# Performance work log

Measured on AMD Instinct MI355X. Metric: run time of the kernel, lower is better.

## Reference

```python
import jax, jax.numpy as jnp
import numpy as np

N = 50000
E = 1600000
F_IN = 503
F_H = 128
NEG_SLOPE = 0.2


def setup_inputs() -> dict:
    key = jax.random.key(0)
    ks = jax.random.split(key, 24)
    s = 0.05
    inp = {
        "x": jax.random.normal(ks[0], (N, F_IN), jnp.float32),
        "edge_index": jax.random.randint(ks[1], (2, E), 0, N, jnp.int64),
        "edge_attr": jax.random.uniform(ks[2], (E, 1), jnp.float32),
        "input_mask": jax.random.uniform(ks[3], (N, 1), jnp.float32),
        # GATConv layer 1 (in=503, out=128, heads=1, edge_dim=1)
        "W1": jax.random.normal(ks[4], (F_IN, F_H), jnp.float32) * s,
        "b1": jnp.zeros((F_H,), jnp.float32),
        "as1": jax.random.normal(ks[5], (F_H,), jnp.float32) * s,
        "ad1": jax.random.normal(ks[6], (F_H,), jnp.float32) * s,
        "We1": jax.random.normal(ks[7], (1, F_H), jnp.float32) * s,
        "ae1": jax.random.normal(ks[8], (F_H,), jnp.float32) * s,
        # GATConv layer 2 (in=128, out=128)
        "W2": jax.random.normal(ks[9], (F_H, F_H), jnp.float32) * s,
        "b2": jnp.zeros((F_H,), jnp.float32),
        "as2": jax.random.normal(ks[10], (F_H,), jnp.float32) * s,
        "ad2": jax.random.normal(ks[11], (F_H,), jnp.float32) * s,
        "We2": jax.random.normal(ks[12], (1, F_H), jnp.float32) * s,
        "ae2": jax.random.normal(ks[13], (F_H,), jnp.float32) * s,
        # edge/node heads
        "Wb": jax.random.normal(ks[14], (F_H, 1), jnp.float32) * s,
        "bb": jnp.zeros((1,), jnp.float32),
        "Ww": jax.random.normal(ks[15], (F_H, 1), jnp.float32) * s,
        "bw": jnp.zeros((1,), jnp.float32),
    }
    return inp


def _gat_conv(x, src, dst, ea, W, b, a_src_vec, a_dst_vec, We, a_edge_vec):
    """PyG GATConv, heads=1, add_self_loops=True, fill_value='mean'."""
    n = x.shape[0]
    loop = jnp.arange(n)
    # self-loop edge attrs = mean of incoming edge attrs (0 if none)
    deg = jax.ops.segment_sum(jnp.ones(dst.shape, ea.dtype), dst, num_segments=n)
    ea_loop = jax.ops.segment_sum(ea, dst, num_segments=n) / jnp.maximum(deg, 1.0)[:, None]
    s = jnp.concatenate([src, loop])
    d = jnp.concatenate([dst, loop])
    ea2 = jnp.concatenate([ea, ea_loop], axis=0)  # [E+N, 1]

    h = x @ W                              # [N, F_H]
    a_s = h @ a_src_vec                    # [N]
    a_d = h @ a_dst_vec                    # [N]
    a_e = (ea2 @ We) @ a_edge_vec          # [E+N]

    alpha = jax.nn.leaky_relu(a_s[s] + a_d[d] + a_e, NEG_SLOPE)
    # scatter-softmax over destination neighborhoods (every node has a self loop)
    m = jax.lax.stop_gradient(jax.ops.segment_max(alpha, d, num_segments=n))
    ex = jnp.exp(alpha - m[d])
    den = jax.ops.segment_sum(ex, d, num_segments=n)
    coef = ex / den[d]                     # [E+N]

    out = jax.ops.segment_sum(coef[:, None] * h[s], d, num_segments=n)
    return out + b


def reference(x, edge_index, edge_attr, input_mask,
              W1, b1, as1, ad1, We1, ae1,
              W2, b2, as2, ad2, We2, ae2,
              Wb, bb, Ww, bw):
    src, dst = edge_index[0], edge_index[1]
    h = jax.nn.relu(_gat_conv(x, src, dst, edge_attr, W1, b1, as1, ad1, We1, ae1))
    h = jax.nn.relu(_gat_conv(h, src, dst, edge_attr, W2, b2, as2, ad2, We2, ae2))
    b_out = (h @ Wb + bb) * input_mask          # [N, 1]
    # directed graph: is_directed() is True, so use all edges
    w = ((h[src] + h[dst]) * 0.5) @ Ww + bw     # [E, 1]
    return (w, b_out)
```

## Files before the change

kernel.cpp:

```cpp
#include <hip/hip_runtime.h>
#include <hip/hip_fp16.h>

#define FH 128
#define NEG_SLOPE 0.2f
#define GBM 64
#define GBK 64

typedef _Float16 f16x8 __attribute__((ext_vector_type(8)));
typedef float f32x4 __attribute__((ext_vector_type(4)));

__global__ void rank_kernel(const int* __restrict__ ei, int* __restrict__ cnt,
                            unsigned short* __restrict__ rank, int E) {
  int e = blockIdx.x * 256 + threadIdx.x;
  if (e >= E) return;
  int dst = ei[E + e];
  rank[e] = (unsigned short)atomicAdd(&cnt[dst], 1);
}

__global__ void scan_blocksum(const int* __restrict__ deg, int* __restrict__ bsum, int n) {
  __shared__ int sm[256];
  int i = blockIdx.x * 256 + threadIdx.x;
  sm[threadIdx.x] = (i < n) ? deg[i] : 0;
  __syncthreads();
  for (int off = 128; off > 0; off >>= 1) {
    if (threadIdx.x < off) sm[threadIdx.x] += sm[threadIdx.x + off];
    __syncthreads();
  }
  if (threadIdx.x == 0) bsum[blockIdx.x] = sm[0];
}

__global__ void scan_bsum(int* __restrict__ bsum, int nb, int* __restrict__ rowptr, int N) {
  __shared__ int sm[1024];
  int t = threadIdx.x;
  int v = (t < nb) ? bsum[t] : 0;
  sm[t] = v;
  __syncthreads();
  for (int off = 1; off < 1024; off <<= 1) {
    int u = (t >= off) ? sm[t - off] : 0;
    __syncthreads();
    sm[t] += u;
    __syncthreads();
  }
  if (t < nb) bsum[t] = sm[t] - v;
  if (t == 1023) rowptr[N] = sm[1023];
}

__global__ void scan_final(const int* __restrict__ deg, const int* __restrict__ bsum,
                           int* __restrict__ rowptr, int n) {
  __shared__ int sm[256];
  int i = blockIdx.x * 256 + threadIdx.x;
  int v = (i < n) ? deg[i] : 0;
  sm[threadIdx.x] = v;
  __syncthreads();
  for (int off = 1; off < 256; off <<= 1) {
    int u = (threadIdx.x >= off) ? sm[threadIdx.x - off] : 0;
    __syncthreads();
    sm[threadIdx.x] += u;
    __syncthreads();
  }
  if (i < n) rowptr[i] = bsum[blockIdx.x] + sm[threadIdx.x] - v;
}

__global__ void place_kernel(const int* __restrict__ ei, const float* __restrict__ ea,
                             const int* __restrict__ rowptr,
                             const unsigned short* __restrict__ rank,
                             unsigned int* __restrict__ pack, int E) {
  int e = blockIdx.x * 256 + threadIdx.x;
  if (e >= E) return;
  int src = ei[e], dst = ei[E + e];
  int pos = rowptr[dst] + rank[e];
  unsigned short h = __half_as_ushort(__float2half(ea[e]));
  pack[pos] = ((unsigned int)src << 16) | h;
}

__global__ void cvec_kernel(const float* __restrict__ We1, const float* __restrict__ ae1,
                            const float* __restrict__ We2, const float* __restrict__ ae2,
                            float* __restrict__ cv) {
  int l = threadIdx.x;
  float s1 = We1[l] * ae1[l] + We1[l + 64] * ae1[l + 64];
  float s2 = We2[l] * ae2[l] + We2[l + 64] * ae2[l + 64];
  for (int off = 32; off; off >>= 1) { s1 += __shfl_down(s1, off); s2 += __shfl_down(s2, off); }
  if (l == 0) { cv[0] = s1; cv[1] = s2; }
}

__global__ void wcvt_kernel(const float* __restrict__ W, __half* __restrict__ Wt,
                            int K, int Kpad) {
  int idx = blockIdx.x * 256 + threadIdx.x;
  if (idx >= 128 * Kpad) return;
  int n = idx / Kpad, k = idx - n * Kpad;
  Wt[idx] = (k < K) ? __float2half(W[(size_t)k * 128 + n]) : __float2half(0.f);
}

__global__ __launch_bounds__(256, 4) void mfma_gemm_kernel(
    const float* __restrict__ X, const __half* __restrict__ Wt_,
    const float* __restrict__ avs, const float* __restrict__ avd,
    __half* __restrict__ H16, float* __restrict__ a_s, float* __restrict__ a_d,
    int M, int K, int Kpad) {
  __shared__ _Float16 Bl[2 * 8 * 64 * 8];
  const _Float16* __restrict__ Wt = (const _Float16*)Wt_;
  const int tid  = threadIdx.x;
  const int lane = tid & 63;
  const int w    = tid >> 6;
  const int m0   = blockIdx.x * GBM;

  f32x4 acc[8];
  #pragma unroll
  for (int i = 0; i < 8; i++) acc[i] = (f32x4){0.f, 0.f, 0.f, 0.f};

  const int arow   = m0 + w * 16 + (lane & 15);
  const int arow_c = arow < M ? arow : (M - 1);
  const float* __restrict__ Xrow = X + (size_t)arow_c * K;
  const int kgrp = (lane >> 4) * 8;

  const int sg = tid & 7, snb = tid >> 3;

  for (int k0 = 0; k0 < Kpad; k0 += GBK) {
    #pragma unroll
    for (int i = 0; i < 4; i++) {
      int n = snb + 32 * i;
      f16x8 v = *(const f16x8*)(Wt + (size_t)n * Kpad + k0 + sg * 8);
      int kt = sg >> 2, nt = n >> 4;
      int fl = (n & 15) + (sg & 3) * 16;
      *(f16x8*)&Bl[((kt * 8 + nt) * 64 + fl) * 8] = v;
    }
    __syncthreads();
    const bool fast = (k0 + GBK <= K);
    #pragma unroll
    for (int kt = 0; kt < 2; kt++) {
      int kb = k0 + kt * 32 + kgrp;
      f16x8 af;
      if (fast) {
        #pragma unroll
        for (int j = 0; j < 8; j++) af[j] = (_Float16)Xrow[kb + j];
      } else {
        #pragma unroll
        for (int j = 0; j < 8; j++)
          af[j] = (kb + j < K) ? (_Float16)Xrow[kb + j] : (_Float16)0.f;
      }
      #pragma unroll
      for (int nt = 0; nt < 8; nt++) {
        f16x8 bf = *(const f16x8*)&Bl[((kt * 8 + nt) * 64 + lane) * 8];
        acc[nt] = __builtin_amdgcn_mfma_f32_16x16x32_f16(af, bf, acc[nt], 0, 0, 0);
      }
    }
    __syncthreads();
  }

  const int rbase = m0 + w * 16 + (lane >> 4) * 4;
  const int col   = lane & 15;
  float as_v[8], ad_v[8];
  #pragma unroll
  for (int nt = 0; nt < 8; nt++) {
    as_v[nt] = avs[nt * 16 + col];
    ad_v[nt] = avd[nt * 16 + col];
  }
  #pragma unroll
  for (int r = 0; r < 4; r++) {
    int gm = rbase + r;
    float ps = 0.f, pd = 0.f;
    #pragma unroll
    for (int nt = 0; nt < 8; nt++) {
      ps += acc[nt][r] * as_v[nt];
      pd += acc[nt][r] * ad_v[nt];
    }
    #pragma unroll
    for (int msk = 1; msk < 16; msk <<= 1) {
      ps += __shfl_xor(ps, msk);
      pd += __shfl_xor(pd, msk);
    }
    if (gm < M) {
      #pragma unroll
      for (int nt = 0; nt < 8; nt++)
        H16[(size_t)gm * FH + nt * 16 + col] = __float2half(acc[nt][r]);
      if (col == 0) { a_s[gm] = ps; a_d[gm] = pd; }
    }
  }
}

__global__ __launch_bounds__(256) void agg_kernel(
    const __half* __restrict__ H16, const int* __restrict__ rowptr,
    const unsigned int* __restrict__ pack,
    const float* __restrict__ a_s, const float* __restrict__ a_d,
    const float* __restrict__ cv, int cidx,
    const float* __restrict__ bias,
    float* __restrict__ Hout, int N) {
  const int node = (blockIdx.x * 256 + threadIdx.x) >> 6;
  const int lane = threadIdx.x & 63;
  const int slot = lane >> 4, sl = lane & 15;
  if (node >= N) return;
  const _Float16* __restrict__ Hh = (const _Float16*)H16;
  const float c   = cv[cidx];
  const float adn = a_d[node];
  const int beg = rowptr[node], end = rowptr[node + 1];

  float acc[8] = {0.f, 0.f, 0.f, 0.f, 0.f, 0.f, 0.f, 0.f};
  float den = 0.f, ea_tot = 0.f;

  for (int p = beg + slot; p < end; p += 4) {
    unsigned w0 = pack[p];
    int s0 = w0 >> 16;
    float e0 = __half2float(__ushort_as_half((unsigned short)(w0 & 0xffff)));
    float al = a_s[s0] + adn + c * e0;
    al = fmaxf(al, NEG_SLOPE * al);
    float ex = __expf(al);
    f16x8 h = *(const f16x8*)(Hh + (size_t)s0 * FH + sl * 8);
    ea_tot += e0;
    den += ex;
    #pragma unroll
    for (int j = 0; j < 8; j++) acc[j] += ex * (float)h[j];
  }
  ea_tot += __shfl_xor(ea_tot, 16); ea_tot += __shfl_xor(ea_tot, 32);
  den    += __shfl_xor(den,    16); den    += __shfl_xor(den,    32);
  #pragma unroll
  for (int j = 0; j < 8; j++) {
    acc[j] += __shfl_xor(acc[j], 16);
    acc[j] += __shfl_xor(acc[j], 32);
  }
  {
    int dg = end - beg;
    float eal = ea_tot / fmaxf((float)dg, 1.f);
    float al = a_s[node] + adn + c * eal;
    al = fmaxf(al, NEG_SLOPE * al);
    float ex = __expf(al);
    f16x8 h = *(const f16x8*)(Hh + (size_t)node * FH + sl * 8);
    den += ex;
    #pragma unroll
    for (int j = 0; j < 8; j++) acc[j] += ex * (float)h[j];
  }
  if (slot == 0) {
    float inv = 1.f / den;
    float4 b0 = *(const float4*)&bias[sl * 8];
    float4 b1 = *(const float4*)&bias[sl * 8 + 4];
    float4 o0, o1;
    o0.x = fmaxf(acc[0] * inv + b0.x, 0.f);
    o0.y = fmaxf(acc[1] * inv + b0.y, 0.f);
    o0.z = fmaxf(acc[2] * inv + b0.z, 0.f);
    o0.w = fmaxf(acc[3] * inv + b0.w, 0.f);
    o1.x = fmaxf(acc[4] * inv + b1.x, 0.f);
    o1.y = fmaxf(acc[5] * inv + b1.y, 0.f);
    o1.z = fmaxf(acc[6] * inv + b1.z, 0.f);
    o1.w = fmaxf(acc[7] * inv + b1.w, 0.f);
    *(float4*)&Hout[(size_t)node * FH + sl * 8]     = o0;
    *(float4*)&Hout[(size_t)node * FH + sl * 8 + 4] = o1;
  }
}

__global__ void node_head_kernel(const float* __restrict__ H, const float* __restrict__ Wb,
                                 const float* __restrict__ bb, const float* __restrict__ Ww,
                                 const float* __restrict__ mask,
                                 float* __restrict__ bout, float* __restrict__ p, int N) {
  int gid = blockIdx.x * 256 + threadIdx.x;
  int node = gid >> 6, lane = threadIdx.x & 63;
  if (node >= N) return;
  float2 h  = *(const float2*)&H[(size_t)node * FH + lane * 2];
  float2 wb = *(const float2*)&Wb[lane * 2];
  float2 ww = *(const float2*)&Ww[lane * 2];
  float sb = h.x * wb.x + h.y * wb.y;
  float sw = h.x * ww.x + h.y * ww.y;
  for (int off = 32; off; off >>= 1) { sb += __shfl_down(sb, off); sw += __shfl_down(sw, off); }
  if (lane == 0) {
    bout[node] = (sb + bb[0]) * mask[node];
    p[node]    = sw;
  }
}

__global__ void edge_head_kernel(const int* __restrict__ ei, const float* __restrict__ p,
                                 const float* __restrict__ bw, float* __restrict__ w, int E) {
  int base = (blockIdx.x * 256 + threadIdx.x) * 4;
  if (base >= E) return;
  float b = bw[0];
  if (base + 4 <= E && (E & 3) == 0) {
    int4 s = *(const int4*)&ei[base];
    int4 d = *(const int4*)&ei[E + base];
    float4 o;
    o.x = 0.5f * (p[s.x] + p[d.x]) + b;
    o.y = 0.5f * (p[s.y] + p[d.y]) + b;
    o.z = 0.5f * (p[s.z] + p[d.z]) + b;
    o.w = 0.5f * (p[s.w] + p[d.w]) + b;
    *(float4*)&w[base] = o;
  } else {
    for (int e = base; e < E && e < base + 4; e++)
      w[e] = 0.5f * (p[ei[e]] + p[ei[E + e]]) + b;
  }
}

extern "C" void kernel_launch(void* const* d_in, const int* in_sizes, int n_in,
                              void* d_out, int out_size, void* d_ws, size_t ws_size,
                              hipStream_t stream) {
  (void)n_in; (void)out_size; (void)ws_size;
  const float* x    = (const float*)d_in[0];
  const int*   ei   = (const int*)  d_in[1];
  const float* ea   = (const float*)d_in[2];
  const float* mask = (const float*)d_in[3];
  const float* W1   = (const float*)d_in[4];
  const float* b1   = (const float*)d_in[5];
  const float* as1  = (const float*)d_in[6];
  const float* ad1  = (const float*)d_in[7];
  const float* We1  = (const float*)d_in[8];
  const float* ae1  = (const float*)d_in[9];
  const float* W2   = (const float*)d_in[10];
  const float* b2   = (const float*)d_in[11];
  const float* as2  = (const float*)d_in[12];
  const float* ad2  = (const float*)d_in[13];
  const float* We2  = (const float*)d_in[14];
  const float* ae2  = (const float*)d_in[15];
  const float* Wb   = (const float*)d_in[16];
  const float* bb   = (const float*)d_in[17];
  const float* Ww   = (const float*)d_in[18];
  const float* bw   = (const float*)d_in[19];

  const int N  = in_sizes[3];
  const int E  = in_sizes[1] / 2;
  const int K1 = in_sizes[0] / N;
  const int K1p = (K1 + GBK - 1) & ~(GBK - 1);

  char* ws = (char*)d_ws;
  size_t off = 0;
  auto alloc = [&](size_t bytes) -> char* {
    char* q = ws + off;
    off = (off + bytes + 255) & ~(size_t)255;
    return q;
  };
  int*   cnt    = (int*)  alloc((size_t)N * 4);
  int*   rowptr = (int*)  alloc((size_t)(N + 1) * 4);
  int*   bsum   = (int*)  alloc(1024 * 4);
  unsigned short* rank = (unsigned short*)alloc((size_t)E * 2);
  unsigned int*   pack = (unsigned int*)  alloc((size_t)E * 4);
  float* a_s    = (float*)alloc((size_t)N * 4);
  float* a_d    = (float*)alloc((size_t)N * 4);
  __half* H16   = (__half*)alloc((size_t)N * FH * 2);
  float* HB     = (float*)alloc((size_t)N * FH * 4);
  float* pbuf   = (float*)alloc((size_t)N * 4);
  float* cv     = (float*)alloc(8);
  __half* W1t   = (__half*)alloc((size_t)FH * K1p * 2);
  __half* W2t   = (__half*)alloc((size_t)FH * FH * 2);

  float* w_out = (float*)d_out;
  float* b_out = (float*)d_out + E;

  hipMemsetAsync(cnt, 0, (size_t)N * 4, stream);

  const int eb  = (E + 255) / 256;
  const int nb  = (N + 255) / 256;
  const int gb  = (N + GBM - 1) / GBM;
  const int wbk = ((size_t)N * 64 + 255) / 256;
  const int ab  = (N + 3) / 4;
  const int ehb = (E + 1023) / 1024;

  rank_kernel  <<<eb, 256, 0, stream>>>(ei, cnt, rank, E);
  scan_blocksum<<<nb, 256, 0, stream>>>(cnt, bsum, N);
  scan_bsum    <<<1, 1024, 0, stream>>>(bsum, nb, rowptr, N);
  scan_final   <<<nb, 256, 0, stream>>>(cnt, bsum, rowptr, N);
  place_kernel <<<eb, 256, 0, stream>>>(ei, ea, rowptr, rank, pack, E);
  cvec_kernel  <<<1, 64, 0, stream>>>(We1, ae1, We2, ae2, cv);
  wcvt_kernel  <<<(128 * K1p + 255) / 256, 256, 0, stream>>>(W1, W1t, K1, K1p);
  wcvt_kernel  <<<(128 * FH + 255) / 256, 256, 0, stream>>>(W2, W2t, FH, FH);

  mfma_gemm_kernel<<<gb, 256, 0, stream>>>(x, W1t, as1, ad1, H16, a_s, a_d, N, K1, K1p);
  agg_kernel  <<<ab, 256, 0, stream>>>(H16, rowptr, pack, a_s, a_d, cv, 0, b1, HB, N);
  mfma_gemm_kernel<<<gb, 256, 0, stream>>>(HB, W2t, as2, ad2, H16, a_s, a_d, N, FH, FH);
  agg_kernel  <<<ab, 256, 0, stream>>>(H16, rowptr, pack, a_s, a_d, cv, 1, b2, HB, N);
  node_head_kernel<<<wbk, 256, 0, stream>>>(HB, Wb, bb, Ww, mask, b_out, pbuf, N);
  edge_head_kernel<<<ehb, 256, 0, stream>>>(ei, pbuf, bw, w_out, E);
}
```

Baseline: 313.4 us.

## Replace global-atomic CSR build with per-block shared-memory histograms and column scan

Builds the destination-sorted edge list with 64 blocks that each histogram their edge slice in LDS using packed 8-bit counters, then a column scan over blocks gives each block's per-node offsets. Placement reuses the same LDS atomics to find each edge's local rank, so the global atomicAdd pass, the rank array and the memset go away. In exchange it adds two NB×N ushort arrays and runs on only 64 blocks. The 8-bit counters assume fewer than 256 edges per node per block, and the 12512-word LDS array caps N at about 50048. The edge head also drops the E%4 condition on its vector path.

```diff
diff --git a/kernel.cpp b/kernel.cpp
--- a/kernel.cpp
+++ b/kernel.cpp
@@ -5,16 +5,54 @@
 #define NEG_SLOPE 0.2f
 #define GBM 64
 #define GBK 64
+#define NB 64
+#define HT 1024
+#define NWMAX 12512
 
 typedef _Float16 f16x8 __attribute__((ext_vector_type(8)));
 typedef float f32x4 __attribute__((ext_vector_type(4)));
 
-__global__ void rank_kernel(const int* __restrict__ ei, int* __restrict__ cnt,
-                            unsigned short* __restrict__ rank, int E) {
-  int e = blockIdx.x * 256 + threadIdx.x;
-  if (e >= E) return;
-  int dst = ei[E + e];
-  rank[e] = (unsigned short)atomicAdd(&cnt[dst], 1);
+__global__ __launch_bounds__(HT) void hist_kernel(const int* __restrict__ ei,
+                                                  unsigned short* __restrict__ hist,
+                                                  int E, int N) {
+  __shared__ unsigned int lh[NWMAX];
+  const int b = blockIdx.x, tid = threadIdx.x;
+  const int nw = (N + 3) >> 2;
+  for (int j = tid; j < nw; j += HT) lh[j] = 0u;
+  __syncthreads();
+  const int Epb = (E + NB - 1) / NB;
+  const int beg = b * Epb, end = min(E, beg + Epb);
+  for (int i = beg + tid; i < end; i += HT) {
+    int d = ei[E + i];
+    atomicAdd(&lh[d >> 2], 1u << ((d & 3) * 8));
+  }
+  __syncthreads();
+  unsigned short* hb = hist + (size_t)b * N;
+  for (int j = tid; j < nw; j += HT) {
+    unsigned v = lh[j];
+    int bin = j * 4;
+    if (bin + 3 < N) {
+      ushort4 o;
+      o.x = v & 255u; o.y = (v >> 8) & 255u; o.z = (v >> 16) & 255u; o.w = v >> 24;
+      *(ushort4*)&hb[bin] = o;
+    } else {
+      for (int k = 0; k < 4 && bin + k < N; k++) hb[bin + k] = (v >> (k * 8)) & 255u;
+    }
+  }
+}
+
+__global__ void colscan_kernel(const unsigned short* __restrict__ hist,
+                               unsigned short* __restrict__ off,
+                               int* __restrict__ cnt, int N) {
+  int bin = blockIdx.x * 256 + threadIdx.x;
+  if (bin >= N) return;
+  int s = 0;
+  for (int b = 0; b < NB; b++) {
+    int t = hist[(size_t)b * N + bin];
+    off[(size_t)b * N + bin] = (unsigned short)s;
+    s += t;
+  }
+  cnt[bin] = s;
 }
 
 __global__ void scan_blocksum(const int* __restrict__ deg, int* __restrict__ bsum, int n) {
@@ -61,16 +99,28 @@
   if (i < n) rowptr[i] = bsum[blockIdx.x] + sm[threadIdx.x] - v;
 }
 
-__global__ void place_kernel(const int* __restrict__ ei, const float* __restrict__ ea,
-                             const int* __restrict__ rowptr,
-                             const unsigned short* __restrict__ rank,
-                             unsigned int* __restrict__ pack, int E) {
-  int e = blockIdx.x * 256 + threadIdx.x;
-  if (e >= E) return;
-  int src = ei[e], dst = ei[E + e];
-  int pos = rowptr[dst] + rank[e];
-  unsigned short h = __half_as_ushort(__float2half(ea[e]));
-  pack[pos] = ((unsigned int)src << 16) | h;
+__global__ __launch_bounds__(HT) void place_kernel(const int* __restrict__ ei,
+                                                   const float* __restrict__ ea,
+                                                   const int* __restrict__ rowptr,
+                                                   const unsigned short* __restrict__ off,
+                                                   unsigned int* __restrict__ pack,
+                                                   int E, int N) {
+  __shared__ unsigned int lc[NWMAX];
+  const int b = blockIdx.x, tid = threadIdx.x;
+  const int nw = (N + 3) >> 2;
+  for (int j = tid; j < nw; j += HT) lc[j] = 0u;
+  __syncthreads();
+  const int Epb = (E + NB - 1) / NB;
+  const int beg = b * Epb, end = min(E, beg + Epb);
+  const unsigned short* __restrict__ ob = off + (size_t)b * N;
+  for (int i = beg + tid; i < end; i += HT) {
+    int d = ei[E + i];
+    unsigned r = atomicAdd(&lc[d >> 2], 1u << ((d & 3) * 8));
+    int local = (r >> ((d & 3) * 8)) & 255;
+    int pos = rowptr[d] + (int)ob[d] + local;
+    unsigned short h = __half_as_ushort(__float2half(ea[i]));
+    pack[pos] = ((unsigned)ei[i] << 16) | h;
+  }
 }
 
 __global__ void cvec_kernel(const float* __restrict__ We1, const float* __restrict__ ae1,
@@ -269,7 +319,7 @@
   int base = (blockIdx.x * 256 + threadIdx.x) * 4;
   if (base >= E) return;
   float b = bw[0];
-  if (base + 4 <= E && (E & 3) == 0) {
+  if (base + 4 <= E) {
     int4 s = *(const int4*)&ei[base];
     int4 d = *(const int4*)&ei[E + base];
     float4 o;
@@ -279,7 +329,7 @@
     o.w = 0.5f * (p[s.w] + p[d.w]) + b;
     *(float4*)&w[base] = o;
   } else {
-    for (int e = base; e < E && e < base + 4; e++)
+    for (int e = base; e < E; e++)
       w[e] = 0.5f * (p[ei[e]] + p[ei[E + e]]) + b;
   }
 }
@@ -315,16 +365,17 @@
   const int K1p = (K1 + GBK - 1) & ~(GBK - 1);
 
   char* ws = (char*)d_ws;
-  size_t off = 0;
+  size_t off0 = 0;
   auto alloc = [&](size_t bytes) -> char* {
-    char* q = ws + off;
-    off = (off + bytes + 255) & ~(size_t)255;
+    char* q = ws + off0;
+    off0 = (off0 + bytes + 255) & ~(size_t)255;
     return q;
   };
   int*   cnt    = (int*)  alloc((size_t)N * 4);
   int*   rowptr = (int*)  alloc((size_t)(N + 1) * 4);
   int*   bsum   = (int*)  alloc(1024 * 4);
-  unsigned short* rank = (unsigned short*)alloc((size_t)E * 2);
+  unsigned short* hist = (unsigned short*)alloc((size_t)NB * N * 2);
+  unsigned short* offb = (unsigned short*)alloc((size_t)NB * N * 2);
   unsigned int*   pack = (unsigned int*)  alloc((size_t)E * 4);
   float* a_s    = (float*)alloc((size_t)N * 4);
   float* a_d    = (float*)alloc((size_t)N * 4);
@@ -338,28 +389,26 @@
   float* w_out = (float*)d_out;
   float* b_out = (float*)d_out + E;
 
-  hipMemsetAsync(cnt, 0, (size_t)N * 4, stream);
-
-  const int eb  = (E + 255) / 256;
   const int nb  = (N + 255) / 256;
   const int gb  = (N + GBM - 1) / GBM;
   const int wbk = ((size_t)N * 64 + 255) / 256;
   const int ab  = (N + 3) / 4;
-  const int ehb = (E + 1023) / 1024;
-
-  rank_kernel  <<<eb, 256, 0, stream>>>(ei, cnt, rank, E);
-  scan_blocksum<<<nb, 256, 0, stream>>>(cnt, bsum, N);
-  scan_bsum    <<<1, 1024, 0, stream>>>(bsum, nb, rowptr, N);
-  scan_final   <<<nb, 256, 0, stream>>>(cnt, bsum, rowptr, N);
-  place_kernel <<<eb, 256, 0, stream>>>(ei, ea, rowptr, rank, pack, E);
-  cvec_kernel  <<<1, 64, 0, stream>>>(We1, ae1, We2, ae2, cv);
-  wcvt_kernel  <<<(128 * K1p + 255) / 256, 256, 0, stream>>>(W1, W1t, K1, K1p);
-  wcvt_kernel  <<<(128 * FH + 255) / 256, 256, 0, stream>>>(W2, W2t, FH, FH);
+  const int eb4 = (E + 1023) / 1024;
+
+  hist_kernel   <<<NB, HT, 0, stream>>>(ei, hist, E, N);
+  colscan_kernel<<<nb, 256, 0, stream>>>(hist, offb, cnt, N);
+  scan_blocksum <<<nb, 256, 0, stream>>>(cnt, bsum, N);
+  scan_bsum     <<<1, 1024, 0, stream>>>(bsum, nb, rowptr, N);
+  scan_final    <<<nb, 256, 0, stream>>>(cnt, bsum, rowptr, N);
+  place_kernel  <<<NB, HT, 0, stream>>>(ei, ea, rowptr, offb, pack, E, N);
+  cvec_kernel   <<<1, 64, 0, stream>>>(We1, ae1, We2, ae2, cv);
+  wcvt_kernel   <<<(128 * K1p + 255) / 256, 256, 0, stream>>>(W1, W1t, K1, K1p);
+  wcvt_kernel   <<<(128 * FH + 255) / 256, 256, 0, stream>>>(W2, W2t, FH, FH);
 
   mfma_gemm_kernel<<<gb, 256, 0, stream>>>(x, W1t, as1, ad1, H16, a_s, a_d, N, K1, K1p);
   agg_kernel  <<<ab, 256, 0, stream>>>(H16, rowptr, pack, a_s, a_d, cv, 0, b1, HB, N);
   mfma_gemm_kernel<<<gb, 256, 0, stream>>>(HB, W2t, as2, ad2, H16, a_s, a_d, N, FH, FH);
   agg_kernel  <<<ab, 256, 0, stream>>>(H16, rowptr, pack, a_s, a_d, cv, 1, b2, HB, N);
   node_head_kernel<<<wbk, 256, 0, stream>>>(HB, Wb, bb, Ww, mask, b_out, pbuf, N);
-  edge_head_kernel<<<ehb, 256, 0, stream>>>(ei, pbuf, bw, w_out, E);
-}
+  edge_head_kernel<<<eb4, 256, 0, stream>>>(ei, pbuf, bw, w_out, E);
+}
```

Result: no change. 317.8 us (+1.4%).
